# Performance work log

Measured on AMD Instinct MI355X. Metric: run time of the kernel, lower is better.

The kernel has to match this reference:

```python
import jax, jax.numpy as jnp
import numpy as np

N = 100000      # nodes
E = 1600000     # graph edges
P = 800000      # hypergraph incidence pairs
HE = 20000      # hyperedges
F_IN = 128      # node features
DIM = 64        # hidden dim (hard-coded in module)
NC = 40         # num_classes


def _lin_init(key, fan_in, fan_out):
    k1, k2 = jax.random.split(key)
    s = 1.0 / np.sqrt(fan_in)
    W = jax.random.uniform(k1, (fan_in, fan_out), jnp.float32, -s, s)
    b = jax.random.uniform(k2, (fan_out,), jnp.float32, -s, s)
    return W, b


def setup_inputs() -> dict:
    key = jax.random.key(0)
    ks = jax.random.split(key, 10)
    x = jax.random.normal(ks[0], (N, F_IN), jnp.float32)
    edge_index = jax.random.randint(ks[1], (2, E), 0, N, dtype=jnp.int64)
    node_idx = jax.random.randint(ks[2], (P,), 0, N, dtype=jnp.int64)
    he_idx = jax.random.randint(ks[3], (P,), 0, HE, dtype=jnp.int64)
    hyperedge_index = jnp.stack([node_idx, he_idx], axis=0)
    W_h1, b_h1 = _lin_init(ks[4], F_IN, DIM)
    W_h2, b_h2 = _lin_init(ks[5], DIM, DIM)
    W_c1, b_c1 = _lin_init(ks[6], F_IN + DIM, DIM)
    W_c2, b_c2 = _lin_init(ks[7], DIM, NC)
    W_lp, b_lp = _lin_init(ks[8], NC, NC)
    return dict(x=x, edge_index=edge_index, hyperedge_index=hyperedge_index,
                W_h1=W_h1, b_h1=b_h1, W_h2=W_h2, b_h2=b_h2,
                W_c1=W_c1, b_c1=b_c1, W_c2=W_c2, b_c2=b_c2,
                W_lp=W_lp, b_lp=b_lp)


def hypergraph_conv(x, node_idx, he_idx, W, b):
    # PyG HypergraphConv (no attention, hyperedge_weight = 1):
    # out = D^{-1} H B^{-1} H^T (x W) + b
    xw = x @ W                                    # [N, D]
    ones = jnp.ones(node_idx.shape[0], xw.dtype)
    Dn = jax.ops.segment_sum(ones, node_idx, num_segments=N)   # node degree
    Bh = jax.ops.segment_sum(ones, he_idx, num_segments=HE)    # hyperedge size
    D_inv = jnp.where(Dn > 0, 1.0 / Dn, 0.0)
    B_inv = jnp.where(Bh > 0, 1.0 / Bh, 0.0)
    # node -> hyperedge: m_e = (1/|e|) sum_{i in e} xw[i]
    msg1 = xw[node_idx] * B_inv[he_idx][:, None]               # [P, D]
    e_feat = jax.ops.segment_sum(msg1, he_idx, num_segments=HE)
    # hyperedge -> node: out_i = (1/deg(i)) sum_{e ni i} m_e
    msg2 = e_feat[he_idx] * D_inv[node_idx][:, None]           # [P, D]
    out = jax.ops.segment_sum(msg2, node_idx, num_segments=N)
    return out + b


def gcn_conv(x, edge_index, W, b):
    # PyG GCNConv: add self-loops, symmetric normalization
    xw = x @ W                                    # [N, D]
    loop = jnp.arange(N, dtype=edge_index.dtype)
    src = jnp.concatenate([edge_index[0], loop])
    dst = jnp.concatenate([edge_index[1], loop])
    deg = jax.ops.segment_sum(jnp.ones(dst.shape[0], xw.dtype), dst, num_segments=N)
    dis = jnp.where(deg > 0, jax.lax.rsqrt(deg), 0.0)
    norm = dis[src] * dis[dst]                    # [E+N]
    out = jax.ops.segment_sum(xw[src] * norm[:, None], dst, num_segments=N)
    return out + b


def reference(x, edge_index, hyperedge_index,
              W_h1, b_h1, W_h2, b_h2, W_c1, b_c1, W_c2, b_c2, W_lp, b_lp):
    node_idx, he_idx = hyperedge_index[0], hyperedge_index[1]
    x_hyper = jax.nn.relu(hypergraph_conv(x, node_idx, he_idx, W_h1, b_h1))
    # dropout is identity in eval mode
    x_hyper = hypergraph_conv(x_hyper, node_idx, he_idx, W_h2, b_h2)
    xc = jnp.concatenate([x, x_hyper], axis=1)    # [N, F_IN + DIM]
    x_gnn = jax.nn.relu(gcn_conv(xc, edge_index, W_c1, b_c1))
    x_gnn = gcn_conv(x_gnn, edge_index, W_c2, b_c2)
    return x_gnn @ W_lp + b_lp                     # [N, NC]
```

## Files before the change

### kernel.cpp

```cpp
#include <hip/hip_runtime.h>
#include <hip/hip_bf16.h>


typedef __attribute__((ext_vector_type(8))) short s16x8;
typedef __attribute__((ext_vector_type(4))) float f32x4;
typedef __attribute__((ext_vector_type(8))) float f32x8;

__device__ __forceinline__ float ldf(const void* p, int f32, long long i) {
    if (f32) return ((const float*)p)[i];
    unsigned v = ((unsigned)((const unsigned short*)p)[i]) << 16;
    return __uint_as_float(v);
}

__device__ __forceinline__ int ldi(const int* __restrict__ w, int i64, long long i, int lim) {
    int v = i64 ? w[2 * i] : w[i];
    return ((unsigned)v < (unsigned)lim) ? v : 0;
}

__device__ __forceinline__ float b2f(unsigned short u) {
    return __uint_as_float(((unsigned)u) << 16);
}
__device__ __forceinline__ unsigned short f2b(float f) {
    __hip_bfloat16 h = __float2bfloat16(f);
    return *reinterpret_cast<unsigned short*>(&h);
}
__device__ __forceinline__ f32x8 b2f8(s16x8 u) {
    f32x8 r;
#pragma unroll
    for (int q = 0; q < 8; q++) r[q] = b2f((unsigned short)u[q]);
    return r;
}
__device__ __forceinline__ s16x8 f2b8(f32x8 v) {
    s16x8 r;
#pragma unroll
    for (int q = 0; q < 8; q++) r[q] = (short)f2b(v[q]);
    return r;
}

__device__ int det_bf16_blk(const void* p, int nbytes, int* shcnt) {
    if (threadIdx.x == 0) *shcnt = 0;
    __syncthreads();
    const unsigned short* u = (const unsigned short*)p;
    int np = nbytes; if (np > 2048) np = 2048;
    int c = 0;
    for (int i = threadIdx.x; i < np; i += blockDim.x) {
        unsigned e = (u[i] >> 7) & 0xFFu;
        if (e != 0u && (e < 90u || e > 160u)) c++;
    }
    atomicAdd(shcnt, c);
    __syncthreads();
    int f = ((*shcnt) * 8 > np) ? 1 : 0;
    __syncthreads();
    return f;
}

__device__ int det_i64_blk(const int* w, int np, int* shcnt) {
    if (threadIdx.x == 0) *shcnt = 0;
    __syncthreads();
    int c = 0;
    for (int i = threadIdx.x; i < np; i += blockDim.x)
        if (w[2 * i + 1] != 0) c++;
    atomicAdd(shcnt, c);
    __syncthreads();
    int f = ((*shcnt) == 0) ? 1 : 0;
    __syncthreads();
    return f;
}

struct BP { const void* B; int nbytes; int K; int M; int Mp; unsigned short* out; };
struct D6 { const void* p[6]; int n[6]; int fi[6]; int i64[6]; };

__global__ void detprep_k(D6 d6, int* __restrict__ FL,
                          int* __restrict__ gBkt, int* __restrict__ done,
                          BP p0, BP p1, BP p2,
                          const void* Wc2, int szWc2, const void* Wlp, int szWlp,
                          const void* bc2, int szbc2, const void* blp, int szblp,
                          unsigned short* __restrict__ btl, float* __restrict__ bias2, int NC) {
    __shared__ int shcnt;
    int b = blockIdx.x, t = threadIdx.x;
    if (b == 0) {
        for (int i = t; i < 768; i += blockDim.x) gBkt[i] = 0;
        if (t == 0) done[0] = 0;
    }
    if (b < 6) {
        int f = d6.i64[b] ? det_i64_blk((const int*)d6.p[b], d6.n[b], &shcnt)
                          : det_bf16_blk(d6.p[b], d6.n[b], &shcnt);
        if (t == 0) FL[d6.fi[b]] = f;
        return;
    }
    if (b < 9) {
        BP p = (b == 6) ? p0 : (b == 7) ? p1 : p2;
        int fb = det_bf16_blk(p.B, p.nbytes, &shcnt);
        int tot = p.Mp * p.K;
        for (int e = t; e < tot; e += blockDim.x) {
            int m = e / p.K, k = e - m * p.K;
            float v = (m < p.M) ? ldf(p.B, fb, (long long)k * p.M + m) : 0.f;
            p.out[e] = f2b(v);
        }
        return;
    }
    int fw2 = det_bf16_blk(Wc2, szWc2, &shcnt);
    int flp = det_bf16_blk(Wlp, szWlp, &shcnt);
    int fb2 = det_bf16_blk(bc2, szbc2, &shcnt);
    int fbl = det_bf16_blk(blp, szblp, &shcnt);
    extern __shared__ float sm[];
    float* sW2 = sm;
    float* sLP = sm + 64 * NC;
    for (int e = t; e < 64 * NC; e += blockDim.x) sW2[e] = ldf(Wc2, fw2, e);
    for (int e = t; e < NC * NC; e += blockDim.x) sLP[e] = ldf(Wlp, flp, e);
    for (int e = t; e < 48 * 64; e += blockDim.x) btl[e] = 0;
    __syncthreads();
    for (int e = t; e < 64 * NC; e += blockDim.x) {
        int r = e / NC, c = e % NC;
        float s = 0.f;
        for (int k = 0; k < NC; k++) s = fmaf(sW2[r * NC + k], sLP[k * NC + c], s);
        btl[c * 64 + r] = f2b(s);
    }
    if (t < NC) {
        float s = ldf(blp, fbl, t);
        for (int k = 0; k < NC; k++) s = fmaf(ldf(bc2, fb2, k), sLP[k * NC + t], s);
        bias2[t] = s;
    }
}

struct Item { int b1; unsigned p1; int b2; unsigned p2; };

__device__ __forceinline__ Item decode(const int* __restrict__ ew, const int* __restrict__ hw,
                                       const int* __restrict__ FL, long long i,
                                       int E, int P, int N, int HE, int shN, int shH) {
    Item it; it.b2 = -1; it.p2 = 0;
    if (i < E) {
        int g = FL[11];
        int key = ldi(ew, g, (long long)E + i, N);
        int val = ldi(ew, g, i, N);
        it.b1 = key >> shN;
        it.p1 = ((unsigned)(key & ((1 << shN) - 1)) << 20) | (unsigned)val;
    } else {
        long long j = i - E;
        int g = FL[12];
        int nd = ldi(hw, g, j, N);
        int he = ldi(hw, g, (long long)P + j, HE);
        it.b1 = 256 + (nd >> shN);
        it.p1 = ((unsigned)(nd & ((1 << shN) - 1)) << 20) | (unsigned)he;
        it.b2 = 512 + (he >> shH);
        it.p2 = ((unsigned)(he & ((1 << shH) - 1)) << 20) | (unsigned)nd;
    }
    return it;
}

#define PCHUNK 8192
#define PTHREADS 1024

__global__ __launch_bounds__(PTHREADS)
void chunkhist_k(const int* __restrict__ ew, const int* __restrict__ hw,
                 const int* __restrict__ FL, int* __restrict__ gcnt,
                 int* __restrict__ chunkHist, int* __restrict__ done,
                 int* __restrict__ bkOff, int* __restrict__ gcur,
                 int E, int P, int N, int HE, int shN, int shH) {
    __shared__ int hist[768];
    int t = threadIdx.x;
    for (int b = t; b < 768; b += PTHREADS) hist[b] = 0;
    __syncthreads();
    long long T = (long long)E + P;
    long long start = (long long)blockIdx.x * PCHUNK;
    long long end = start + PCHUNK; if (end > T) end = T;
    for (long long i = start + t; i < end; i += PTHREADS) {
        Item it = decode(ew, hw, FL, i, E, P, N, HE, shN, shH);
        atomicAdd(&hist[it.b1], 1);
        if (it.b2 >= 0) atomicAdd(&hist[it.b2], 1);
    }
    __syncthreads();
    long long hbase = (long long)blockIdx.x * 768;
    for (int b = t; b < 768; b += PTHREADS) {
        int h = hist[b];
        chunkHist[hbase + b] = h;
        if (h) atomicAdd(&gcnt[b], h);
    }
    __syncthreads();
    __shared__ int isLast;
    if (t == 0) {
        __threadfence();
        isLast = (atomicAdd(done, 1) == (int)gridDim.x - 1);
    }
    __syncthreads();
    if (!isLast) return;
    __shared__ int sh[256];
    for (int c = 0; c < 3; c++) {
        int v = 0;
        if (t < 256) { v = atomicAdd(&gcnt[c * 256 + t], 0); sh[t] = v; }
        __syncthreads();
        for (int o = 1; o < 256; o <<= 1) {
            int y = (t < 256 && t >= o) ? sh[t - o] : 0;
            __syncthreads();
            if (t < 256) sh[t] += y;
            __syncthreads();
        }
        if (t < 256) {
            int excl = sh[t] - v;
            bkOff[c * 256 + t] = excl;
            long long rb = (c == 0) ? 0 : ((c == 1) ? (long long)E : (long long)E + P);
            gcur[c * 256 + t] = (int)(rb + excl);
        }
        __syncthreads();
    }
}

__global__ __launch_bounds__(PTHREADS)
void place_k(const int* __restrict__ ew, const int* __restrict__ hw,
             const int* __restrict__ FL, int* __restrict__ gcur,
             const int* __restrict__ chunkHist, unsigned* __restrict__ pbuf,
             int E, int P, int N, int HE, int shN, int shH) {
    __shared__ int cur[768];
    long long T = (long long)E + P;
    long long start = (long long)blockIdx.x * PCHUNK;
    long long end = start + PCHUNK; if (end > T) end = T;
    int t = threadIdx.x;
    long long hbase = (long long)blockIdx.x * 768;
    for (int b = t; b < 768; b += PTHREADS) {
        int h = chunkHist[hbase + b];
        cur[b] = h ? atomicAdd(&gcur[b], h) : 0;
    }
    __syncthreads();
    for (long long i = start + t; i < end; i += PTHREADS) {
        Item it = decode(ew, hw, FL, i, E, P, N, HE, shN, shH);
        int s1 = atomicAdd(&cur[it.b1], 1);
        pbuf[s1] = it.p1;
        if (it.b2 >= 0) {
            int s2 = atomicAdd(&cur[it.b2], 1);
            pbuf[s2] = it.p2;
        }
    }
}

__global__ void build_k(const unsigned* __restrict__ pbuf,
                        const int* __restrict__ gcnt, const int* __restrict__ bkOff,
                        int* __restrict__ eoff, int* __restrict__ ecnt, int* __restrict__ esrc,
                        int* __restrict__ poffN, int* __restrict__ pcntN, int* __restrict__ pheL,
                        int* __restrict__ poffH, int* __restrict__ pcntH, int* __restrict__ pniL,
                        float* __restrict__ dis, float* __restrict__ Dinv, float* __restrict__ Binv,
                        int E, int P, int N, int HE, int shN, int shH) {
    __shared__ int hist[512];
    __shared__ int offs[512];
    __shared__ int s2[256];
    int b = blockIdx.x, t = threadIdx.x;
    int csr = b >> 8, lb = b & 255;
    int sh    = (csr == 2) ? shH : shN;
    int nkeys = (csr == 2) ? HE : N;
    int span = 1 << sh;
    int keyBase = lb << sh;
    if (keyBase >= nkeys) return;
    int keyEnd = keyBase + span; if (keyEnd > nkeys) keyEnd = nkeys;
    int cnt = gcnt[b];
    long long rbase = (csr == 0) ? 0 : ((csr == 1) ? (long long)E : (long long)E + P);
    long long pstart = rbase + bkOff[b];
    int lstBase = bkOff[b];
    int* off  = (csr == 0) ? eoff : ((csr == 1) ? poffN : poffH);
    int* cntA = (csr == 0) ? ecnt : ((csr == 1) ? pcntN : pcntH);
    int* lst  = (csr == 0) ? esrc : ((csr == 1) ? pheL : pniL);

    for (int k = t; k < 512; k += 256) hist[k] = 0;
    __syncthreads();
    for (int i = t; i < cnt; i += 256)
        atomicAdd(&hist[pbuf[pstart + i] >> 20], 1);
    __syncthreads();
    int a0 = hist[2 * t], a1 = hist[2 * t + 1];
    s2[t] = a0 + a1;
    __syncthreads();
    for (int o = 1; o < 256; o <<= 1) {
        int y = (t >= o) ? s2[t - o] : 0;
        __syncthreads();
        s2[t] += y;
        __syncthreads();
    }
    int excl = s2[t] - (a0 + a1);
    offs[2 * t] = excl;
    offs[2 * t + 1] = excl + a0;
    __syncthreads();
    for (int k = keyBase + t; k < keyEnd; k += 256) {
        int h = hist[k - keyBase];
        off[k]  = lstBase + offs[k - keyBase];
        cntA[k] = h;
        if (csr == 0)      dis[k]  = rsqrtf((float)(h + 1));
        else if (csr == 1) Dinv[k] = h ? (1.f / (float)h) : 0.f;
        else               Binv[k] = h ? (1.f / (float)h) : 0.f;
    }
    __syncthreads();
    for (int i = t; i < cnt; i += 256) {
        unsigned u = pbuf[pstart + i];
        int lk = u >> 20;
        int slot = atomicAdd(&offs[lk], 1);
        lst[lstBase + slot] = (int)(u & 0xFFFFFu);
    }
}

__global__ void gat_n2e_k(const unsigned short* __restrict__ xw, const int* __restrict__ off,
                          const int* __restrict__ cnt, const int* __restrict__ lst,
                          const float* __restrict__ Binv, unsigned short* __restrict__ ef, int HE) {
    int idx = blockIdx.x * blockDim.x + threadIdx.x;
    int e = idx >> 3, l = idx & 7;
    if (e >= HE) return;
    int o = off[e], c = cnt[e];
    f32x8 a = {0.f, 0.f, 0.f, 0.f, 0.f, 0.f, 0.f, 0.f};
    int j = 0;
    for (; j + 4 <= c; j += 4) {
        int s0 = lst[o + j], s1 = lst[o + j + 1], s2 = lst[o + j + 2], s3 = lst[o + j + 3];
        f32x8 v0 = b2f8(*(const s16x8*)&xw[((long long)s0 << 6) + l * 8]);
        f32x8 v1 = b2f8(*(const s16x8*)&xw[((long long)s1 << 6) + l * 8]);
        f32x8 v2 = b2f8(*(const s16x8*)&xw[((long long)s2 << 6) + l * 8]);
        f32x8 v3 = b2f8(*(const s16x8*)&xw[((long long)s3 << 6) + l * 8]);
#pragma unroll
        for (int q = 0; q < 8; q++) a[q] += (v0[q] + v1[q]) + (v2[q] + v3[q]);
    }
    for (; j < c; j++) {
        f32x8 v = b2f8(*(const s16x8*)&xw[((long long)lst[o + j] << 6) + l * 8]);
#pragma unroll
        for (int q = 0; q < 8; q++) a[q] += v[q];
    }
    float bi = Binv[e];
#pragma unroll
    for (int q = 0; q < 8; q++) a[q] *= bi;
    *(s16x8*)&ef[((long long)e << 6) + l * 8] = f2b8(a);
}

template <bool RELU>
__global__ void gat_e2n_k(const unsigned short* __restrict__ ef, const int* __restrict__ off,
                          const int* __restrict__ cnt, const int* __restrict__ lst,
                          const float* __restrict__ Dinv, const void* __restrict__ bias,
                          const int* __restrict__ fb, unsigned short* __restrict__ out, int N) {
    int idx = blockIdx.x * blockDim.x + threadIdx.x;
    int w = idx >> 3, l = idx & 7;
    if (w >= N) return;
    int o = off[w], c = cnt[w];
    f32x8 a = {0.f, 0.f, 0.f, 0.f, 0.f, 0.f, 0.f, 0.f};
    int j = 0;
    for (; j + 4 <= c; j += 4) {
        int s0 = lst[o + j], s1 = lst[o + j + 1], s2 = lst[o + j + 2], s3 = lst[o + j + 3];
        f32x8 v0 = b2f8(*(const s16x8*)&ef[((long long)s0 << 6) + l * 8]);
        f32x8 v1 = b2f8(*(const s16x8*)&ef[((long long)s1 << 6) + l * 8]);
        f32x8 v2 = b2f8(*(const s16x8*)&ef[((long long)s2 << 6) + l * 8]);
        f32x8 v3 = b2f8(*(const s16x8*)&ef[((long long)s3 << 6) + l * 8]);
#pragma unroll
        for (int q = 0; q < 8; q++) a[q] += (v0[q] + v1[q]) + (v2[q] + v3[q]);
    }
    for (; j < c; j++) {
        f32x8 v = b2f8(*(const s16x8*)&ef[((long long)lst[o + j] << 6) + l * 8]);
#pragma unroll
        for (int q = 0; q < 8; q++) a[q] += v[q];
    }
    float di = Dinv[w];
    int fbv = fb[0];
#pragma unroll
    for (int q = 0; q < 8; q++) {
        float bq = ldf(bias, fbv, l * 8 + q);
        a[q] = a[q] * di + bq;
        if (RELU) a[q] = fmaxf(a[q], 0.f);
    }
    *(s16x8*)&out[((long long)w << 6) + l * 8] = f2b8(a);
}

template <bool RELU>
__global__ void gcn_gat_k(const unsigned short* __restrict__ y, const int* __restrict__ off,
                          const int* __restrict__ cnt, const int* __restrict__ lst,
                          const float* __restrict__ dis, const void* __restrict__ bias,
                          const int* __restrict__ fb, unsigned short* __restrict__ out, int N) {
    int idx = blockIdx.x * blockDim.x + threadIdx.x;
    int w = idx >> 3, l = idx & 7;
    if (w >= N) return;
    int o = off[w], c = cnt[w];
    f32x8 a = b2f8(*(const s16x8*)&y[((long long)w << 6) + l * 8]);
    int j = 0;
    for (; j + 4 <= c; j += 4) {
        int s0 = lst[o + j], s1 = lst[o + j + 1], s2 = lst[o + j + 2], s3 = lst[o + j + 3];
        f32x8 v0 = b2f8(*(const s16x8*)&y[((long long)s0 << 6) + l * 8]);
        f32x8 v1 = b2f8(*(const s16x8*)&y[((long long)s1 << 6) + l * 8]);
        f32x8 v2 = b2f8(*(const s16x8*)&y[((long long)s2 << 6) + l * 8]);
        f32x8 v3 = b2f8(*(const s16x8*)&y[((long long)s3 << 6) + l * 8]);
#pragma unroll
        for (int q = 0; q < 8; q++) a[q] += (v0[q] + v1[q]) + (v2[q] + v3[q]);
    }
    for (; j < c; j++) {
        f32x8 v = b2f8(*(const s16x8*)&y[((long long)lst[o + j] << 6) + l * 8]);
#pragma unroll
        for (int q = 0; q < 8; q++) a[q] += v[q];
    }
    float dd = dis[w];
    int fbv = fb[0];
#pragma unroll
    for (int q = 0; q < 8; q++) {
        float bq = ldf(bias, fbv, l * 8 + q);
        a[q] = a[q] * dd + bq;
        if (RELU) a[q] = fmaxf(a[q], 0.f);
    }
    *(s16x8*)&out[((long long)w << 6) + l * 8] = f2b8(a);
}

__global__ void gcn_gatM_k(const unsigned short* __restrict__ y2, const int* __restrict__ off,
                           const int* __restrict__ cnt, const int* __restrict__ lst,
                           const float* __restrict__ dis, const float* __restrict__ bias2,
                           float4* __restrict__ out4, int N, int NC) {
    int idx = blockIdx.x * blockDim.x + threadIdx.x;
    int wave = idx >> 6, l64 = idx & 63;
    int lpr = NC >> 3;
    int rpw = 64 / lpr;
    int grp = l64 / lpr, li = l64 - grp * lpr;
    int w = wave * rpw + grp;
    if (grp >= rpw || w >= N) return;
    int o = off[w], c = cnt[w];
    f32x8 a = b2f8(*(const s16x8*)&y2[(long long)w * NC + li * 8]);
    int j = 0;
    for (; j + 4 <= c; j += 4) {
        int s0 = lst[o + j], s1 = lst[o + j + 1], s2 = lst[o + j + 2], s3 = lst[o + j + 3];
        f32x8 v0 = b2f8(*(const s16x8*)&y2[(long long)s0 * NC + li * 8]);
        f32x8 v1 = b2f8(*(const s16x8*)&y2[(long long)s1 * NC + li * 8]);
        f32x8 v2 = b2f8(*(const s16x8*)&y2[(long long)s2 * NC + li * 8]);
        f32x8 v3 = b2f8(*(const s16x8*)&y2[(long long)s3 * NC + li * 8]);
#pragma unroll
        for (int q = 0; q < 8; q++) a[q] += (v0[q] + v1[q]) + (v2[q] + v3[q]);
    }
    for (; j < c; j++) {
        f32x8 v = b2f8(*(const s16x8*)&y2[(long long)lst[o + j] * NC + li * 8]);
#pragma unroll
        for (int q = 0; q < 8; q++) a[q] += v[q];
    }
    float dd = dis[w];
    const float4* b4 = (const float4*)&bias2[li * 8];
    float4 b0 = b4[0], b1 = b4[1];
    float4 lo = make_float4(a[0] * dd + b0.x, a[1] * dd + b0.y, a[2] * dd + b0.z, a[3] * dd + b0.w);
    float4 hi = make_float4(a[4] * dd + b1.x, a[5] * dd + b1.y, a[6] * dd + b1.z, a[7] * dd + b1.w);
    long long base = ((long long)w * NC + li * 8) >> 2;
    out4[base] = lo;
    out4[base + 1] = hi;
}

__device__ __forceinline__ s16x8 load8bf(const void* A, int af, long long base) {
    s16x8 o;
    if (af) {
        float4 v0 = *(const float4*)((const float*)A + base);
        float4 v1 = *(const float4*)((const float*)A + base + 4);
        o[0] = (short)f2b(v0.x); o[1] = (short)f2b(v0.y);
        o[2] = (short)f2b(v0.z); o[3] = (short)f2b(v0.w);
        o[4] = (short)f2b(v1.x); o[5] = (short)f2b(v1.y);
        o[6] = (short)f2b(v1.z); o[7] = (short)f2b(v1.w);
    } else {
        o = *(const s16x8*)&((const unsigned short*)A)[base];
    }
    return o;
}

template <int KK, int MM, bool CATMODE, bool ABF16, bool SCALE>
__global__ __launch_bounds__(256)
void gemm_mfma2_k(const void* __restrict__ A, const int* __restrict__ fA,
                  const unsigned short* __restrict__ A2,
                  const unsigned short* __restrict__ Bt,
                  const float* __restrict__ dscale,
                  unsigned short* __restrict__ C, int NR) {
    constexpr int MT = (MM + 15) / 16;
    static_assert(KK % 32 == 0, "K must be multiple of 32");

    const int t = threadIdx.x;
    const int wid = t >> 6, lane = t & 63;
    const long long r0 = ((long long)blockIdx.x * 4 + wid) * 32;
    if (r0 >= NR) return;

    const int af = fA ? fA[0] : 1;
    const int arow = lane & 15;
    const int kgrp = lane >> 4;
    long long ra = r0 + arow;      if (ra > NR - 1) ra = NR - 1;
    long long rb = r0 + 16 + arow; if (rb > NR - 1) rb = NR - 1;

    f32x4 acc0[MT] = {};
    f32x4 acc1[MT] = {};
#pragma unroll
    for (int kc = 0; kc < KK; kc += 32) {
        const int kb = kc + kgrp * 8;
        s16x8 a0, a1;
        if constexpr (CATMODE) {
            if (kc < 128) {
                a0 = load8bf(A, af, ra * 128 + kb);
                a1 = load8bf(A, af, rb * 128 + kb);
            } else {
                a0 = *(const s16x8*)&A2[ra * 64 + (kb - 128)];
                a1 = *(const s16x8*)&A2[rb * 64 + (kb - 128)];
            }
        } else if constexpr (ABF16) {
            a0 = *(const s16x8*)&((const unsigned short*)A)[ra * KK + kb];
            a1 = *(const s16x8*)&((const unsigned short*)A)[rb * KK + kb];
        } else {
            a0 = load8bf(A, af, ra * (long long)KK + kb);
            a1 = load8bf(A, af, rb * (long long)KK + kb);
        }
#pragma unroll
        for (int m = 0; m < MT; m++) {
            s16x8 b = *(const s16x8*)&Bt[(m * 16 + arow) * KK + kb];
            acc0[m] = __builtin_amdgcn_mfma_f32_16x16x32_bf16(a0, b, acc0[m], 0, 0, 0);
            acc1[m] = __builtin_amdgcn_mfma_f32_16x16x32_bf16(a1, b, acc1[m], 0, 0, 0);
        }
    }

    const int col0 = lane & 15;
    const int rsub = (lane >> 4) * 4;
#pragma unroll
    for (int h = 0; h < 2; h++) {
#pragma unroll
        for (int i = 0; i < 4; i++) {
            long long r = r0 + h * 16 + rsub + i;
            if (r < NR) {
                float s = SCALE ? dscale[r] : 1.f;
#pragma unroll
                for (int m = 0; m < MT; m++) {
                    int col = m * 16 + col0;
                    float val = h ? acc1[m][i] : acc0[m][i];
                    if (MT * 16 == MM || col < MM)
                        C[r * MM + col] = f2b(val * s);
                }
            }
        }
    }
}

static inline dim3 g1d(long long n, int b) { return dim3((unsigned)((n + b - 1) / b)); }
static inline int imin(int a, int b) { return a < b ? a : b; }

extern "C" void kernel_launch(void* const* d_in, const int* in_sizes, int n_in,
                              void* d_out, int out_size, void* d_ws, size_t ws_size,
                              hipStream_t stream) {
    const int N  = in_sizes[0] / 128;
    const int E  = in_sizes[1] / 2;
    const int P  = in_sizes[2] / 2;
    const int HE = 20000;
    const int NC = in_sizes[9] / 64;

    const void* x    = d_in[0];
    const int*  ew   = (const int*)d_in[1];
    const int*  hw   = (const int*)d_in[2];
    const void* W_h1 = d_in[3];
    const void* b_h1 = d_in[4];
    const void* W_h2 = d_in[5];
    const void* b_h2 = d_in[6];
    const void* W_c1 = d_in[7];
    const void* b_c1 = d_in[8];
    const void* W_c2 = d_in[9];
    const void* b_c2 = d_in[10];
    const void* W_lp = d_in[11];
    const void* b_lp = d_in[12];

    int shN = 0; while (((N - 1) >> shN) >= 256) shN++;
    int shH = 0; while (((HE - 1) >> shH) >= 256) shH++;

    long long T = (long long)E + P;
    int nChunks = (int)((T + PCHUNK - 1) / PCHUNK);

    char* wp = (char*)d_ws;
    auto allocF = [&](size_t n) { float* p = (float*)wp; wp += n * 4; return p; };
    auto allocI = [&](size_t n) { int* p = (int*)wp; wp += n * 4; return p; };
    unsigned short* ub  = (unsigned short*)allocF((size_t)N * 32);
    unsigned short* hb  = (unsigned short*)allocF((size_t)N * 32);
    unsigned short* efb = (unsigned short*)allocF((size_t)HE * 32);
    float* dis   = allocF(N);
    float* Dinv  = allocF(N);
    float* Binv  = allocF(HE);
    float* bias2 = allocF(NC);
    unsigned short* bt1 = (unsigned short*)allocF((size_t)64 * 128 / 2);
    unsigned short* bt2 = (unsigned short*)allocF((size_t)64 * 64 / 2);
    unsigned short* btc = (unsigned short*)allocF((size_t)64 * 192 / 2);
    unsigned short* btl = (unsigned short*)allocF((size_t)48 * 64 / 2);
    int* ecnt  = allocI(N);
    int* pcntN = allocI(N);
    int* pcntH = allocI(HE);
    int* eoff  = allocI(N);
    int* poffN = allocI(N);
    int* poffH = allocI(HE);
    int* esrc  = allocI(E);
    int* pheL  = allocI(P);
    int* pniL  = allocI(P);
    int* gBkt  = allocI(768);
    int* bkOff = allocI(768);
    int* gcur  = allocI(768);
    int* FL    = allocI(16);
    int* done  = allocI(4);
    int* chunkHist = allocI((size_t)nChunks * 768);
    unsigned* pbuf = (unsigned*)allocI((size_t)E + 2 * (size_t)P);

    dim3 b256(256), b1024(PTHREADS), d1(1);

    {
        D6 d6;
        d6.p[0] = x;    d6.n[0] = in_sizes[0];        d6.fi[0] = 0;  d6.i64[0] = 0;
        d6.p[1] = b_h1; d6.n[1] = in_sizes[4];        d6.fi[1] = 2;  d6.i64[1] = 0;
        d6.p[2] = b_h2; d6.n[2] = in_sizes[6];        d6.fi[2] = 4;  d6.i64[2] = 0;
        d6.p[3] = b_c1; d6.n[3] = in_sizes[8];        d6.fi[3] = 6;  d6.i64[3] = 0;
        d6.p[4] = ew;   d6.n[4] = imin(E, 1024);      d6.fi[4] = 11; d6.i64[4] = 1;
        d6.p[5] = hw;   d6.n[5] = imin(P, 1024);      d6.fi[5] = 12; d6.i64[5] = 1;
        BP p0 = {W_h1, in_sizes[3], 128, 64, 64, bt1};
        BP p1 = {W_h2, in_sizes[5],  64, 64, 64, bt2};
        BP p2 = {W_c1, in_sizes[7], 192, 64, 64, btc};
        detprep_k<<<dim3(10), b256, (64 * NC + NC * NC) * 4, stream>>>(
            d6, FL, gBkt, done, p0, p1, p2,
            W_c2, in_sizes[9], W_lp, in_sizes[11],
            b_c2, in_sizes[10], b_lp, in_sizes[12],
            btl, bias2, NC);
    }
    const int* fX   = FL + 0;
    const int* fbh1 = FL + 2;
    const int* fbh2 = FL + 4;
    const int* fbc1 = FL + 6;

    chunkhist_k<<<dim3(nChunks), b1024, 0, stream>>>(ew, hw, FL, gBkt, chunkHist, done,
                                                     bkOff, gcur, E, P, N, HE, shN, shH);
    place_k<<<dim3(nChunks), b1024, 0, stream>>>(ew, hw, FL, gcur, chunkHist, pbuf,
                                                 E, P, N, HE, shN, shH);
    build_k<<<dim3(768), b256, 0, stream>>>(pbuf, gBkt, bkOff,
                                            eoff, ecnt, esrc,
                                            poffN, pcntN, pheL,
                                            poffH, pcntH, pniL,
                                            dis, Dinv, Binv,
                                            E, P, N, HE, shN, shH);

    const dim3 mfmaGrid((N + 127) / 128);
    const dim3 gatN8(g1d((long long)N * 8, 256));
    const dim3 gatH8(g1d((long long)HE * 8, 256));
    const int rpw = 64 / (NC >> 3);
    const dim3 gatNC(g1d((long long)((N + rpw - 1) / rpw) * 64, 256));

    gemm_mfma2_k<128, 64, false, false, false><<<mfmaGrid, b256, 0, stream>>>(
        x, fX, nullptr, bt1, nullptr, ub, N);
    gat_n2e_k<<<gatH8, b256, 0, stream>>>(ub, poffH, pcntH, pniL, Binv, efb, HE);
    gat_e2n_k<true><<<gatN8, b256, 0, stream>>>(efb, poffN, pcntN, pheL, Dinv, b_h1, fbh1, hb, N);

    gemm_mfma2_k<64, 64, false, true, false><<<mfmaGrid, b256, 0, stream>>>(
        hb, nullptr, nullptr, bt2, nullptr, ub, N);
    gat_n2e_k<<<gatH8, b256, 0, stream>>>(ub, poffH, pcntH, pniL, Binv, efb, HE);
    gat_e2n_k<false><<<gatN8, b256, 0, stream>>>(efb, poffN, pcntN, pheL, Dinv, b_h2, fbh2, hb, N);

    gemm_mfma2_k<192, 64, true, false, true><<<mfmaGrid, b256, 0, stream>>>(
        x, fX, hb, btc, dis, ub, N);
    gcn_gat_k<true><<<gatN8, b256, 0, stream>>>(ub, eoff, ecnt, esrc, dis, b_c1, fbc1, hb, N);

    gemm_mfma2_k<64, 40, false, true, true><<<mfmaGrid, b256, 0, stream>>>(
        hb, nullptr, nullptr, btl, dis, ub, N);
    gcn_gatM_k<<<gatNC, b256, 0, stream>>>(ub, eoff, ecnt, esrc, dis, bias2, (float4*)d_out, N, NC);
}
```

Baseline: 417.2 us.

## Reorder second hypergraph conv to aggregate before GEMM and unroll gathers by eight

The second hypergraph layer now aggregates node features to hyperedges first and applies the 64x64 weight to the 20K hyperedge rows instead of the 100K node rows. This is valid because the aggregation is linear and the weight commutes with it. The GEMM work for that layer shrinks about fivefold, at the cost of an extra bf16 rounding at a different point in the computation. All gather kernels also move to a shared helper that unrolls the neighbour loop by eight, giving more loads in flight at the cost of higher register pressure.

```diff
diff --git a/kernel.cpp b/kernel.cpp
--- a/kernel.cpp
+++ b/kernel.cpp
@@ -293,29 +293,50 @@
     }
 }
 
+__device__ __forceinline__ f32x8 gsum64(const unsigned short* __restrict__ src,
+                                        const int* __restrict__ lst,
+                                        int o, int c, int l, f32x8 a) {
+    int j = 0;
+    for (; j + 8 <= c; j += 8) {
+        int s0 = lst[o + j], s1 = lst[o + j + 1], s2 = lst[o + j + 2], s3 = lst[o + j + 3];
+        int s4 = lst[o + j + 4], s5 = lst[o + j + 5], s6 = lst[o + j + 6], s7 = lst[o + j + 7];
+        f32x8 v0 = b2f8(*(const s16x8*)&src[((long long)s0 << 6) + l * 8]);
+        f32x8 v1 = b2f8(*(const s16x8*)&src[((long long)s1 << 6) + l * 8]);
+        f32x8 v2 = b2f8(*(const s16x8*)&src[((long long)s2 << 6) + l * 8]);
+        f32x8 v3 = b2f8(*(const s16x8*)&src[((long long)s3 << 6) + l * 8]);
+        f32x8 v4 = b2f8(*(const s16x8*)&src[((long long)s4 << 6) + l * 8]);
+        f32x8 v5 = b2f8(*(const s16x8*)&src[((long long)s5 << 6) + l * 8]);
+        f32x8 v6 = b2f8(*(const s16x8*)&src[((long long)s6 << 6) + l * 8]);
+        f32x8 v7 = b2f8(*(const s16x8*)&src[((long long)s7 << 6) + l * 8]);
+#pragma unroll
+        for (int q = 0; q < 8; q++)
+            a[q] += ((v0[q] + v1[q]) + (v2[q] + v3[q])) + ((v4[q] + v5[q]) + (v6[q] + v7[q]));
+    }
+    for (; j + 4 <= c; j += 4) {
+        int s0 = lst[o + j], s1 = lst[o + j + 1], s2 = lst[o + j + 2], s3 = lst[o + j + 3];
+        f32x8 v0 = b2f8(*(const s16x8*)&src[((long long)s0 << 6) + l * 8]);
+        f32x8 v1 = b2f8(*(const s16x8*)&src[((long long)s1 << 6) + l * 8]);
+        f32x8 v2 = b2f8(*(const s16x8*)&src[((long long)s2 << 6) + l * 8]);
+        f32x8 v3 = b2f8(*(const s16x8*)&src[((long long)s3 << 6) + l * 8]);
+#pragma unroll
+        for (int q = 0; q < 8; q++) a[q] += (v0[q] + v1[q]) + (v2[q] + v3[q]);
+    }
+    for (; j < c; j++) {
+        f32x8 v = b2f8(*(const s16x8*)&src[((long long)lst[o + j] << 6) + l * 8]);
+#pragma unroll
+        for (int q = 0; q < 8; q++) a[q] += v[q];
+    }
+    return a;
+}
+
 __global__ void gat_n2e_k(const unsigned short* __restrict__ xw, const int* __restrict__ off,
                           const int* __restrict__ cnt, const int* __restrict__ lst,
                           const float* __restrict__ Binv, unsigned short* __restrict__ ef, int HE) {
     int idx = blockIdx.x * blockDim.x + threadIdx.x;
     int e = idx >> 3, l = idx & 7;
     if (e >= HE) return;
-    int o = off[e], c = cnt[e];
     f32x8 a = {0.f, 0.f, 0.f, 0.f, 0.f, 0.f, 0.f, 0.f};
-    int j = 0;
-    for (; j + 4 <= c; j += 4) {
-        int s0 = lst[o + j], s1 = lst[o + j + 1], s2 = lst[o + j + 2], s3 = lst[o + j + 3];
-        f32x8 v0 = b2f8(*(const s16x8*)&xw[((long long)s0 << 6) + l * 8]);
-        f32x8 v1 = b2f8(*(const s16x8*)&xw[((long long)s1 << 6) + l * 8]);
-        f32x8 v2 = b2f8(*(const s16x8*)&xw[((long long)s2 << 6) + l * 8]);
-        f32x8 v3 = b2f8(*(const s16x8*)&xw[((long long)s3 << 6) + l * 8]);
-#pragma unroll
-        for (int q = 0; q < 8; q++) a[q] += (v0[q] + v1[q]) + (v2[q] + v3[q]);
-    }
-    for (; j < c; j++) {
-        f32x8 v = b2f8(*(const s16x8*)&xw[((long long)lst[o + j] << 6) + l * 8]);
-#pragma unroll
-        for (int q = 0; q < 8; q++) a[q] += v[q];
-    }
+    a = gsum64(xw, lst, off[e], cnt[e], l, a);
     float bi = Binv[e];
 #pragma unroll
     for (int q = 0; q < 8; q++) a[q] *= bi;
@@ -330,23 +351,8 @@
     int idx = blockIdx.x * blockDim.x + threadIdx.x;
     int w = idx >> 3, l = idx & 7;
     if (w >= N) return;
-    int o = off[w], c = cnt[w];
     f32x8 a = {0.f, 0.f, 0.f, 0.f, 0.f, 0.f, 0.f, 0.f};
-    int j = 0;
-    for (; j + 4 <= c; j += 4) {
-        int s0 = lst[o + j], s1 = lst[o + j + 1], s2 = lst[o + j + 2], s3 = lst[o + j + 3];
-        f32x8 v0 = b2f8(*(const s16x8*)&ef[((long long)s0 << 6) + l * 8]);
-        f32x8 v1 = b2f8(*(const s16x8*)&ef[((long long)s1 << 6) + l * 8]);
-        f32x8 v2 = b2f8(*(const s16x8*)&ef[((long long)s2 << 6) + l * 8]);
-        f32x8 v3 = b2f8(*(const s16x8*)&ef[((long long)s3 << 6) + l * 8]);
-#pragma unroll
-        for (int q = 0; q < 8; q++) a[q] += (v0[q] + v1[q]) + (v2[q] + v3[q]);
-    }
-    for (; j < c; j++) {
-        f32x8 v = b2f8(*(const s16x8*)&ef[((long long)lst[o + j] << 6) + l * 8]);
-#pragma unroll
-        for (int q = 0; q < 8; q++) a[q] += v[q];
-    }
+    a = gsum64(ef, lst, off[w], cnt[w], l, a);
     float di = Dinv[w];
     int fbv = fb[0];
 #pragma unroll
@@ -366,23 +372,8 @@
     int idx = blockIdx.x * blockDim.x + threadIdx.x;
     int w = idx >> 3, l = idx & 7;
     if (w >= N) return;
-    int o = off[w], c = cnt[w];
     f32x8 a = b2f8(*(const s16x8*)&y[((long long)w << 6) + l * 8]);
-    int j = 0;
-    for (; j + 4 <= c; j += 4) {
-        int s0 = lst[o + j], s1 = lst[o + j + 1], s2 = lst[o + j + 2], s3 = lst[o + j + 3];
-        f32x8 v0 = b2f8(*(const s16x8*)&y[((long long)s0 << 6) + l * 8]);
-        f32x8 v1 = b2f8(*(const s16x8*)&y[((long long)s1 << 6) + l * 8]);
-        f32x8 v2 = b2f8(*(const s16x8*)&y[((long long)s2 << 6) + l * 8]);
-        f32x8 v3 = b2f8(*(const s16x8*)&y[((long long)s3 << 6) + l * 8]);
-#pragma unroll
-        for (int q = 0; q < 8; q++) a[q] += (v0[q] + v1[q]) + (v2[q] + v3[q]);
-    }
-    for (; j < c; j++) {
-        f32x8 v = b2f8(*(const s16x8*)&y[((long long)lst[o + j] << 6) + l * 8]);
-#pragma unroll
-        for (int q = 0; q < 8; q++) a[q] += v[q];
-    }
+    a = gsum64(y, lst, off[w], cnt[w], l, a);
     float dd = dis[w];
     int fbv = fb[0];
 #pragma unroll
@@ -408,6 +399,21 @@
     int o = off[w], c = cnt[w];
     f32x8 a = b2f8(*(const s16x8*)&y2[(long long)w * NC + li * 8]);
     int j = 0;
+    for (; j + 8 <= c; j += 8) {
+        int s0 = lst[o + j], s1 = lst[o + j + 1], s2 = lst[o + j + 2], s3 = lst[o + j + 3];
+        int s4 = lst[o + j + 4], s5 = lst[o + j + 5], s6 = lst[o + j + 6], s7 = lst[o + j + 7];
+        f32x8 v0 = b2f8(*(const s16x8*)&y2[(long long)s0 * NC + li * 8]);
+        f32x8 v1 = b2f8(*(const s16x8*)&y2[(long long)s1 * NC + li * 8]);
+        f32x8 v2 = b2f8(*(const s16x8*)&y2[(long long)s2 * NC + li * 8]);
+        f32x8 v3 = b2f8(*(const s16x8*)&y2[(long long)s3 * NC + li * 8]);
+        f32x8 v4 = b2f8(*(const s16x8*)&y2[(long long)s4 * NC + li * 8]);
+        f32x8 v5 = b2f8(*(const s16x8*)&y2[(long long)s5 * NC + li * 8]);
+        f32x8 v6 = b2f8(*(const s16x8*)&y2[(long long)s6 * NC + li * 8]);
+        f32x8 v7 = b2f8(*(const s16x8*)&y2[(long long)s7 * NC + li * 8]);
+#pragma unroll
+        for (int q = 0; q < 8; q++)
+            a[q] += ((v0[q] + v1[q]) + (v2[q] + v3[q])) + ((v4[q] + v5[q]) + (v6[q] + v7[q]));
+    }
     for (; j + 4 <= c; j += 4) {
         int s0 = lst[o + j], s1 = lst[o + j + 1], s2 = lst[o + j + 2], s3 = lst[o + j + 3];
         f32x8 v0 = b2f8(*(const s16x8*)&y2[(long long)s0 * NC + li * 8]);
@@ -616,27 +622,28 @@
                                             dis, Dinv, Binv,
                                             E, P, N, HE, shN, shH);
 
-    const dim3 mfmaGrid((N + 127) / 128);
+    const dim3 mfmaGridN((N + 127) / 128);
+    const dim3 mfmaGridH((HE + 127) / 128);
     const dim3 gatN8(g1d((long long)N * 8, 256));
     const dim3 gatH8(g1d((long long)HE * 8, 256));
     const int rpw = 64 / (NC >> 3);
     const dim3 gatNC(g1d((long long)((N + rpw - 1) / rpw) * 64, 256));
 
-    gemm_mfma2_k<128, 64, false, false, false><<<mfmaGrid, b256, 0, stream>>>(
+    gemm_mfma2_k<128, 64, false, false, false><<<mfmaGridN, b256, 0, stream>>>(
         x, fX, nullptr, bt1, nullptr, ub, N);
     gat_n2e_k<<<gatH8, b256, 0, stream>>>(ub, poffH, pcntH, pniL, Binv, efb, HE);
     gat_e2n_k<true><<<gatN8, b256, 0, stream>>>(efb, poffN, pcntN, pheL, Dinv, b_h1, fbh1, hb, N);
 
-    gemm_mfma2_k<64, 64, false, true, false><<<mfmaGrid, b256, 0, stream>>>(
-        hb, nullptr, nullptr, bt2, nullptr, ub, N);
-    gat_n2e_k<<<gatH8, b256, 0, stream>>>(ub, poffH, pcntH, pniL, Binv, efb, HE);
-    gat_e2n_k<false><<<gatN8, b256, 0, stream>>>(efb, poffN, pcntN, pheL, Dinv, b_h2, fbh2, hb, N);
-
-    gemm_mfma2_k<192, 64, true, false, true><<<mfmaGrid, b256, 0, stream>>>(
+    gat_n2e_k<<<gatH8, b256, 0, stream>>>(hb, poffH, pcntH, pniL, Binv, efb, HE);
+    gemm_mfma2_k<64, 64, false, true, false><<<mfmaGridH, b256, 0, stream>>>(
+        efb, nullptr, nullptr, bt2, nullptr, ub, HE);
+    gat_e2n_k<false><<<gatN8, b256, 0, stream>>>(ub, poffN, pcntN, pheL, Dinv, b_h2, fbh2, hb, N);
+
+    gemm_mfma2_k<192, 64, true, false, true><<<mfmaGridN, b256, 0, stream>>>(
         x, fX, hb, btc, dis, ub, N);
     gcn_gat_k<true><<<gatN8, b256, 0, stream>>>(ub, eoff, ecnt, esrc, dis, b_c1, fbc1, hb, N);
 
-    gemm_mfma2_k<64, 40, false, true, true><<<mfmaGrid, b256, 0, stream>>>(
+    gemm_mfma2_k<64, 40, false, true, true><<<mfmaGridN, b256, 0, stream>>>(
         hb, nullptr, nullptr, btl, dis, ub, N);
     gcn_gatM_k<<<gatNC, b256, 0, stream>>>(ub, eoff, ecnt, esrc, dis, bias2, (float4*)d_out, N, NC);
 }
```

Result: no change. 410.5 us, median of 2 (-1.6%).
